# Optimization experiments

Measured on AMD Instinct MI355X. Metric: run time of the kernel, lower is better.

The kernel has to match this reference:

```python
import jax, jax.numpy as jnp
import numpy as np

T = 4096
MOL = 2048
DESC = 6
NSOL = 5
H = 2048
D_BLOCK = MOL + DESC            # 2054
FUSE = D_BLOCK * (1 + NSOL)     # 12324
D_IN = FUSE + 1                 # 12325
BOUNDARY_RF = 0.5
CLAMP_LO, CLAMP_HI = 1e-4, 1.0 - 1e-4


def setup_inputs() -> dict:
    key = jax.random.key(0)
    ks = jax.random.split(key, 32)
    s = 0.02  # weight init scale for numerical stability
    d = {
        "mol_vec": jax.random.normal(ks[0], (MOL,), jnp.float32),
        "solvent_seq": jax.random.uniform(ks[1], (T, NSOL), jnp.float32),
        "desc_seq": jax.random.normal(ks[2], (T, DESC), jnp.float32),
        "rf_true": jax.random.uniform(ks[3], (T,), jnp.float32),
        "solvent_vecs": jax.random.normal(ks[4], (NSOL, MOL), jnp.float32),
    }
    wshapes = [
        ("Wf0", (H, D_IN)), ("Wf1", (H, H)), ("Wf2", (H, H)), ("Wof", (1, H)),
        ("Wb0", (H, D_IN)), ("Wb1", (H, H)), ("Wb2", (H, H)), ("Wob", (1, H)),
    ]
    for i, (name, shp) in enumerate(wshapes):
        d[name] = jax.random.normal(ks[5 + i], shp, jnp.float32) * s
    for name, shp in [("bf0", (H,)), ("bf1", (H,)), ("bf2", (H,)), ("bof", (1,)),
                      ("bb0", (H,)), ("bb1", (H,)), ("bb2", (H,)), ("bob", (1,))]:
        d[name] = jnp.zeros(shp, jnp.float32)
    return d


def _step_features(mol_vec, solvent_seq, desc_seq, solvent_vecs):
    # mol_vec [MOL]; solvent_seq [T,NSOL]; desc_seq [T,DESC]; solvent_vecs [NSOL,MOL]
    mol_cat = jnp.concatenate(
        [jnp.broadcast_to(mol_vec, (T, MOL)), desc_seq], axis=-1)  # [T, D_BLOCK]
    scaled = solvent_seq[:, :, None] * solvent_vecs[None, :, :]      # [T,NSOL,MOL]
    sol_block = jnp.concatenate(
        [scaled, jnp.broadcast_to(desc_seq[:, None, :], (T, NSOL, DESC))], axis=-1)
    sol_flat = sol_block.reshape(T, NSOL * D_BLOCK)
    return jnp.concatenate([mol_cat, sol_flat], axis=-1)             # [T, FUSE]


def _trunk(x, W0, b0, W1, b1, W2, b2):
    # 3 Linear+GELU blocks (dropout is identity in eval)
    h = jax.nn.gelu(x @ W0.T + b0, approximate=False)
    h = jax.nn.gelu(h @ W1.T + b1, approximate=False)
    h = jax.nn.gelu(h @ W2.T + b2, approximate=False)
    return h


def reference(mol_vec, solvent_seq, desc_seq, rf_true, solvent_vecs,
              Wf0, bf0, Wf1, bf1, Wf2, bf2, Wof, bof,
              Wb0, bb0, Wb1, bb1, Wb2, bb2, Wob, bob):
    x = _step_features(mol_vec, solvent_seq, desc_seq, solvent_vecs)  # [T, FUSE]
    rf = jax.lax.stop_gradient(rf_true)  # teacher signal is detached
    b = jnp.asarray([BOUNDARY_RF], dtype=x.dtype)
    prev = jnp.concatenate([b, rf[:-1]])  # fwd branch sees rf_true[t-1]
    nxt = jnp.concatenate([rf[1:], b])    # bwd branch sees rf_true[t+1]

    inp_f = jnp.concatenate([x, prev[:, None]], axis=-1)  # [T, D_IN]
    inp_b = jnp.concatenate([x, nxt[:, None]], axis=-1)

    hf = _trunk(inp_f, Wf0, bf0, Wf1, bf1, Wf2, bf2)
    hb = _trunk(inp_b, Wb0, bb0, Wb1, bb1, Wb2, bb2)
    rf_fwd = (hf @ Wof.T + bof).squeeze(-1)  # [T]
    rf_bwd = (hb @ Wob.T + bob).squeeze(-1)
    rf_fwd = jnp.clip(rf_fwd, CLAMP_LO, CLAMP_HI)
    rf_bwd = jnp.clip(rf_bwd, CLAMP_LO, CLAMP_HI)
    return rf_fwd, rf_bwd
```

## Files before the change

### kernel.cpp

```cpp
#include <hip/hip_runtime.h>
#include <hip/hip_fp16.h>
#include <math.h>

#define T_DIM 4096
#define MOL_N 2048
#define DESC_N 6
#define NSOL_N 5
#define H_DIM 2048
#define DBLK 2054
#define D_IN_N 12325
#define GK 2048

typedef _Float16 f16x8 __attribute__((ext_vector_type(8)));
typedef float f32x4 __attribute__((ext_vector_type(4)));

__device__ __forceinline__ float gelu_f(float x) {
    float v = x * (1.5957691f + 0.0713548f * x * x);
    float e = __expf(-v);
    return x / (1.0f + e);
}

__global__ __launch_bounds__(256) void prep_kernel(
    const float* __restrict__ W1f, const float* __restrict__ W2f,
    const float* __restrict__ W1b, const float* __restrict__ W2b,
    _Float16* __restrict__ Wc,
    const float* __restrict__ W0f, const float* __restrict__ W0b,
    const float* __restrict__ b0f, const float* __restrict__ b0b,
    const float* __restrict__ mol, const float* __restrict__ sv,
    float* __restrict__ fold_f, float* __restrict__ fold_b)
{
    __shared__ float red[4][6];
    const int bid = blockIdx.x;
    const int tid = threadIdx.x;

    if (bid < 16384) {
        const int z = bid >> 12;
        const float* __restrict__ src = (z == 0) ? W1f : (z == 1) ? W2f : (z == 2) ? W1b : W2b;
        _Float16* __restrict__ dst = Wc + (size_t)z * H_DIM * H_DIM;
        const int idx = (bid & 4095) * 256 + tid;
        float4 v = ((const float4*)src)[idx];
        struct h4 { _Float16 a, b, c, d; };
        h4 o;
        o.a = (_Float16)v.x; o.b = (_Float16)v.y; o.c = (_Float16)v.z; o.d = (_Float16)v.w;
        ((h4*)dst)[idx] = o;
        return;
    }

    const int fb = bid - 16384;
    const int h = fb & 2047;
    const int z = fb >> 11;
    const float* __restrict__ W0 = z ? W0b : W0f;
    const float* __restrict__ b0 = z ? b0b : b0f;
    float* __restrict__ fold = z ? fold_b : fold_f;
    const float* __restrict__ row = W0 + (size_t)h * D_IN_N;

    float acc[6] = {0.f, 0.f, 0.f, 0.f, 0.f, 0.f};
    #pragma unroll
    for (int i = 0; i < 8; ++i) {
        const int c = tid + i * 256;
        const float m = mol[c];
        acc[0] += row[c] * m;
        #pragma unroll
        for (int s = 0; s < NSOL_N; ++s)
            acc[1 + s] += row[DBLK * (s + 1) + c] * sv[s * MOL_N + c];
    }
    #pragma unroll
    for (int i = 0; i < 6; ++i) {
        float v = acc[i];
        #pragma unroll
        for (int off = 32; off >= 1; off >>= 1)
            v += __shfl_xor(v, off, 64);
        acc[i] = v;
    }
    const int lane = tid & 63, wave = tid >> 6;
    if (lane == 0) {
        #pragma unroll
        for (int i = 0; i < 6; ++i) red[wave][i] = acc[i];
    }
    __syncthreads();
    if (tid < 6) {
        float s = red[0][tid] + red[1][tid] + red[2][tid] + red[3][tid];
        if (tid == 0) fold[h] = s + b0[h];
        else fold[(size_t)tid * H_DIM + h] = s;
    }
    if (tid >= 64 && tid < 70) {
        int j = tid - 64;
        float w = row[MOL_N + j];
        #pragma unroll
        for (int s = 0; s < NSOL_N; ++s) w += row[DBLK * (s + 1) + MOL_N + j];
        fold[(size_t)(6 + j) * H_DIM + h] = w;
    }
    if (tid == 70) fold[(size_t)12 * H_DIM + h] = row[D_IN_N - 1];
}

__global__ __launch_bounds__(256) void h0_kernel(
    const float* __restrict__ fold_f, const float* __restrict__ fold_b,
    const float* __restrict__ desc, const float* __restrict__ sol,
    const float* __restrict__ rf,
    _Float16* __restrict__ h0f, _Float16* __restrict__ h0b)
{
    const int z = blockIdx.z;
    const float* __restrict__ fold = z ? fold_b : fold_f;
    _Float16* __restrict__ h0 = z ? h0b : h0f;
    const int h = blockIdx.x * 256 + threadIdx.x;
    const int tbase = blockIdx.y * 64;

    const float c0 = fold[h];
    float u[NSOL_N], wd[DESC_N];
    #pragma unroll
    for (int s = 0; s < NSOL_N; ++s) u[s] = fold[(size_t)(1 + s) * H_DIM + h];
    #pragma unroll
    for (int j = 0; j < DESC_N; ++j) wd[j] = fold[(size_t)(6 + j) * H_DIM + h];
    const float wp = fold[(size_t)12 * H_DIM + h];

    for (int i = 0; i < 64; ++i) {
        const int t = tbase + i;
        float pv;
        if (z == 0) pv = (t == 0) ? 0.5f : rf[t - 1];
        else        pv = (t == T_DIM - 1) ? 0.5f : rf[t + 1];
        float pre = c0 + wp * pv;
        #pragma unroll
        for (int s = 0; s < NSOL_N; ++s) pre += u[s] * sol[t * NSOL_N + s];
        #pragma unroll
        for (int j = 0; j < DESC_N; ++j) pre += wd[j] * desc[t * DESC_N + j];
        h0[(size_t)t * H_DIM + h] = (_Float16)gelu_f(pre);
    }
}

__device__ __forceinline__ void gemm_core256(
    const _Float16* __restrict__ A, const _Float16* __restrict__ W,
    const int m0, const int n0, char* sc, f32x4 (&acc)[8][4])
{
    const int tid = threadIdx.x;
    const int wave = tid >> 6;
    const int lane = tid & 63;
    const int t15 = lane & 15;
    const int quad = lane >> 4;
    const int wr = wave >> 2;
    const int wc = wave & 3;
    const int poff = (quad ^ ((t15 >> 1) & 3)) * 16;
    const int aoff0 = (wr * 128 + t15) * 64 + poff;
    const int boff0 = 16384 + (wc * 64 + t15) * 64 + poff;

    const _Float16* gsrc[4];
    #pragma unroll
    for (int ld = 0; ld < 4; ++ld) {
        const int j = (ld & 1) * 512 + tid;
        const int r = j >> 2;
        const int c = (j & 3) ^ ((r >> 1) & 3);
        gsrc[ld] = ((ld < 2) ? (A + (size_t)(m0 + r) * GK)
                             : (W + (size_t)(n0 + r) * GK)) + c * 8;
    }

    #pragma unroll
    for (int mi = 0; mi < 8; ++mi)
        #pragma unroll
        for (int ni = 0; ni < 4; ++ni)
            acc[mi][ni] = (f32x4){0.f, 0.f, 0.f, 0.f};

#define STAGE_T(kt, b) do { \
    char* _db = sc + (b) * 32768; \
    const int _ko = (kt) * 32; \
    __builtin_amdgcn_global_load_lds((const __attribute__((address_space(1))) void*)(gsrc[0] + _ko), (__attribute__((address_space(3))) void*)(_db + wave * 1024), 16, 0, 0); \
    __builtin_amdgcn_global_load_lds((const __attribute__((address_space(1))) void*)(gsrc[1] + _ko), (__attribute__((address_space(3))) void*)(_db + 8192 + wave * 1024), 16, 0, 0); \
    __builtin_amdgcn_global_load_lds((const __attribute__((address_space(1))) void*)(gsrc[2] + _ko), (__attribute__((address_space(3))) void*)(_db + 16384 + wave * 1024), 16, 0, 0); \
    __builtin_amdgcn_global_load_lds((const __attribute__((address_space(1))) void*)(gsrc[3] + _ko), (__attribute__((address_space(3))) void*)(_db + 24576 + wave * 1024), 16, 0, 0); \
} while (0)

#define COMPUTE_T(b) do { \
    const char* _db = sc + (b) * 32768; \
    f16x8 aF[8], bF[4]; \
    _Pragma("unroll") \
    for (int mi = 0; mi < 8; ++mi) aF[mi] = *(const f16x8*)(_db + aoff0 + mi * 1024); \
    _Pragma("unroll") \
    for (int ni = 0; ni < 4; ++ni) bF[ni] = *(const f16x8*)(_db + boff0 + ni * 1024); \
    __builtin_amdgcn_s_setprio(1); \
    _Pragma("unroll") \
    for (int mi = 0; mi < 8; ++mi) { \
        _Pragma("unroll") \
        for (int ni = 0; ni < 4; ++ni) \
            acc[mi][ni] = __builtin_amdgcn_mfma_f32_16x16x32_f16(aF[mi], bF[ni], acc[mi][ni], 0, 0, 0); \
    } \
    __builtin_amdgcn_s_setprio(0); \
    asm volatile("s_waitcnt lgkmcnt(0)" ::: "memory"); \
} while (0)

    STAGE_T(0, 0); STAGE_T(1, 1); STAGE_T(2, 2);

    #pragma unroll 1
    for (int k4 = 0; k4 < 60; k4 += 4) {
        asm volatile("s_waitcnt vmcnt(8)" ::: "memory");
        __builtin_amdgcn_s_barrier();
        STAGE_T(k4 + 3, 3); COMPUTE_T(0);
        asm volatile("s_waitcnt vmcnt(8)" ::: "memory");
        __builtin_amdgcn_s_barrier();
        STAGE_T(k4 + 4, 0); COMPUTE_T(1);
        asm volatile("s_waitcnt vmcnt(8)" ::: "memory");
        __builtin_amdgcn_s_barrier();
        STAGE_T(k4 + 5, 1); COMPUTE_T(2);
        asm volatile("s_waitcnt vmcnt(8)" ::: "memory");
        __builtin_amdgcn_s_barrier();
        STAGE_T(k4 + 6, 2); COMPUTE_T(3);
    }
    asm volatile("s_waitcnt vmcnt(8)" ::: "memory");
    __builtin_amdgcn_s_barrier();
    STAGE_T(63, 3); COMPUTE_T(0);
    asm volatile("s_waitcnt vmcnt(8)" ::: "memory");
    __builtin_amdgcn_s_barrier();
    COMPUTE_T(1);
    asm volatile("s_waitcnt vmcnt(4)" ::: "memory");
    __builtin_amdgcn_s_barrier();
    COMPUTE_T(2);
    asm volatile("s_waitcnt vmcnt(0)" ::: "memory");
    __builtin_amdgcn_s_barrier();
    COMPUTE_T(3);

#undef STAGE_T
#undef COMPUTE_T
}

__global__ __launch_bounds__(512, 2) void gemm1_kernel(
    const _Float16* __restrict__ Af, const _Float16* __restrict__ Ab,
    const _Float16* __restrict__ Wfp, const _Float16* __restrict__ Wbp,
    const float* __restrict__ bfp, const float* __restrict__ bbp,
    _Float16* __restrict__ Cf, _Float16* __restrict__ Cb)
{
    __shared__ _Float16 smem[65536];
    char* sc = (char*)smem;
    const int bid = blockIdx.x;
    const int xcd = bid & 7;
    const int slot = bid >> 3;
    const int z = xcd & 1;
    const int q = xcd >> 1;
    const int m0 = (q * 4 + (slot & 3)) * 256;
    const int n0 = (slot >> 2) * 256;

    const _Float16* __restrict__ A = z ? Ab : Af;
    const _Float16* __restrict__ W = z ? Wbp : Wfp;
    const float* __restrict__ bias = z ? bbp : bfp;
    _Float16* __restrict__ C = z ? Cb : Cf;

    f32x4 acc[8][4];
    gemm_core256(A, W, m0, n0, sc, acc);

    const int tid = threadIdx.x;
    const int wave = tid >> 6, lane = tid & 63;
    const int colC = lane & 15, quad = lane >> 4;
    const int wr = wave >> 2, wc = wave & 3;
    #pragma unroll
    for (int ni = 0; ni < 4; ++ni) {
        const int n = n0 + wc * 64 + ni * 16 + colC;
        const float bv = bias[n];
        #pragma unroll
        for (int mi = 0; mi < 8; ++mi) {
            const int mb = m0 + wr * 128 + mi * 16 + quad * 4;
            #pragma unroll
            for (int r = 0; r < 4; ++r)
                C[(size_t)(mb + r) * H_DIM + n] = (_Float16)gelu_f(acc[mi][ni][r] + bv);
        }
    }
}

__global__ __launch_bounds__(512, 2) void gemm_out_kernel(
    const _Float16* __restrict__ Af, const _Float16* __restrict__ Ab,
    const _Float16* __restrict__ Wfp, const _Float16* __restrict__ Wbp,
    const float* __restrict__ bfp, const float* __restrict__ bbp,
    const float* __restrict__ Wof, const float* __restrict__ Wob,
    float* __restrict__ partial)
{
    __shared__ _Float16 smem[65536];
    char* sc = (char*)smem;
    const int bid = blockIdx.x;
    const int xcd = bid & 7;
    const int slot = bid >> 3;
    const int z = xcd & 1;
    const int q = xcd >> 1;
    const int m0 = (q * 4 + (slot & 3)) * 256;
    const int n0 = (slot >> 2) * 256;

    const _Float16* __restrict__ A = z ? Ab : Af;
    const _Float16* __restrict__ W = z ? Wbp : Wfp;
    const float* __restrict__ bias = z ? bbp : bfp;
    const float* __restrict__ Wo = z ? Wob : Wof;

    f32x4 acc[8][4];
    gemm_core256(A, W, m0, n0, sc, acc);

    const int tid = threadIdx.x;
    const int wave = tid >> 6, lane = tid & 63;
    const int colC = lane & 15, quad = lane >> 4;
    const int wr = wave >> 2, wc = wave & 3;

    float bv[4], wo[4];
    #pragma unroll
    for (int ni = 0; ni < 4; ++ni) {
        const int n = n0 + wc * 64 + ni * 16 + colC;
        bv[ni] = bias[n];
        wo[ni] = Wo[n];
    }

    __syncthreads();
    float* red = (float*)sc;
    #pragma unroll
    for (int mi = 0; mi < 8; ++mi) {
        #pragma unroll
        for (int r = 0; r < 4; ++r) {
            float s = 0.f;
            #pragma unroll
            for (int ni = 0; ni < 4; ++ni)
                s += gelu_f(acc[mi][ni][r] + bv[ni]) * wo[ni];
            s += __shfl_xor(s, 1, 64);
            s += __shfl_xor(s, 2, 64);
            s += __shfl_xor(s, 4, 64);
            s += __shfl_xor(s, 8, 64);
            if (colC == 0)
                red[wc * 256 + wr * 128 + mi * 16 + quad * 4 + r] = s;
        }
    }
    __syncthreads();
    if (tid < 256) {
        float v = red[tid] + red[256 + tid] + red[512 + tid] + red[768 + tid];
        const int n_tile = slot >> 2;
        partial[((size_t)z * 8 + n_tile) * T_DIM + m0 + tid] = v;
    }
}

__global__ __launch_bounds__(256) void finalize_kernel(
    const float* __restrict__ partial,
    const float* __restrict__ bof, const float* __restrict__ bob,
    float* __restrict__ out)
{
    const int idx = blockIdx.x * 256 + threadIdx.x;
    const int z = idx >> 12;
    const int row = idx & 4095;
    float v = z ? bob[0] : bof[0];
    #pragma unroll
    for (int nt = 0; nt < 8; ++nt)
        v += partial[((size_t)z * 8 + nt) * T_DIM + row];
    v = fminf(fmaxf(v, 1e-4f), 1.0f - 1e-4f);
    out[idx] = v;
}

extern "C" void kernel_launch(void* const* d_in, const int* in_sizes, int n_in,
                              void* d_out, int out_size, void* d_ws, size_t ws_size,
                              hipStream_t stream)
{
    (void)in_sizes; (void)n_in; (void)out_size; (void)ws_size;
    const float* mol = (const float*)d_in[0];
    const float* sol = (const float*)d_in[1];
    const float* desc = (const float*)d_in[2];
    const float* rf  = (const float*)d_in[3];
    const float* sv  = (const float*)d_in[4];
    const float* Wf0 = (const float*)d_in[5];
    const float* Wf1 = (const float*)d_in[6];
    const float* Wf2 = (const float*)d_in[7];
    const float* Wof = (const float*)d_in[8];
    const float* Wb0 = (const float*)d_in[9];
    const float* Wb1 = (const float*)d_in[10];
    const float* Wb2 = (const float*)d_in[11];
    const float* Wob = (const float*)d_in[12];
    const float* bf0 = (const float*)d_in[13];
    const float* bf1 = (const float*)d_in[14];
    const float* bf2 = (const float*)d_in[15];
    const float* bof = (const float*)d_in[16];
    const float* bb0 = (const float*)d_in[17];
    const float* bb1 = (const float*)d_in[18];
    const float* bb2 = (const float*)d_in[19];
    const float* bob = (const float*)d_in[20];
    float* out = (float*)d_out;

    char* ws = (char*)d_ws;
    float* fold_f = (float*)(ws + 0);
    float* fold_b = (float*)(ws + 131072);
    _Float16* Wc = (_Float16*)(ws + 262144);
    const size_t WSZ = (size_t)H_DIM * H_DIM;
    _Float16* W1f_c = Wc;
    _Float16* W2f_c = Wc + WSZ;
    _Float16* W1b_c = Wc + 2 * WSZ;
    _Float16* W2b_c = Wc + 3 * WSZ;
    const size_t HSZ = (size_t)T_DIM * H_DIM;
    _Float16* h0f = (_Float16*)(ws + 33816576);
    _Float16* h0b = h0f + HSZ;
    _Float16* h1f = (_Float16*)(ws + 33816576 + 2 * 16777216);
    _Float16* h1b = h1f + HSZ;
    float* partial = (float*)(ws + 33816576);

    prep_kernel<<<dim3(20480), 256, 0, stream>>>(
        Wf1, Wf2, Wb1, Wb2, Wc, Wf0, Wb0, bf0, bb0, mol, sv, fold_f, fold_b);
    h0_kernel<<<dim3(8, 64, 2), 256, 0, stream>>>(fold_f, fold_b, desc, sol, rf, h0f, h0b);
    gemm1_kernel<<<dim3(256), 512, 0, stream>>>(h0f, h0b, W1f_c, W1b_c, bf1, bb1, h1f, h1b);
    gemm_out_kernel<<<dim3(256), 512, 0, stream>>>(h1f, h1b, W2f_c, W2b_c, bf2, bb2, Wof, Wob, partial);
    finalize_kernel<<<dim3(32), 256, 0, stream>>>(partial, bof, bob, out);
}
```

Baseline: 465.8 us.

## Split prep into LDS-staged W0 fold kernel and separate fp16 convert kernel

The combined prep kernel is split in two. A fold kernel streams each W0 row into LDS using global_load_lds with 16-byte chunks, handling rows of 12325 floats that are not 16-byte aligned, and processes four rows per block. A separate convert kernel casts W1/W2 to fp16 with four float4 loads per thread. The h0 kernel now computes four hidden units per thread, using vectorized fold loads and 4-wide fp16 stores. The goal is better load coalescing and more memory-level parallelism in these bandwidth-bound preprocessing stages, at the cost of one extra kernel launch and 53KB of LDS per fold block, which limits occupancy.

```diff
diff --git a/kernel.cpp b/kernel.cpp
--- a/kernel.cpp
+++ b/kernel.cpp
@@ -20,77 +20,103 @@
     return x / (1.0f + e);
 }
 
-__global__ __launch_bounds__(256) void prep_kernel(
-    const float* __restrict__ W1f, const float* __restrict__ W2f,
-    const float* __restrict__ W1b, const float* __restrict__ W2b,
-    _Float16* __restrict__ Wc,
+__global__ __launch_bounds__(256) void fold2_kernel(
     const float* __restrict__ W0f, const float* __restrict__ W0b,
     const float* __restrict__ b0f, const float* __restrict__ b0b,
     const float* __restrict__ mol, const float* __restrict__ sv,
     float* __restrict__ fold_f, float* __restrict__ fold_b)
 {
+    __shared__ float wrow[13312];
     __shared__ float red[4][6];
-    const int bid = blockIdx.x;
     const int tid = threadIdx.x;
-
-    if (bid < 16384) {
-        const int z = bid >> 12;
-        const float* __restrict__ src = (z == 0) ? W1f : (z == 1) ? W2f : (z == 2) ? W1b : W2b;
-        _Float16* __restrict__ dst = Wc + (size_t)z * H_DIM * H_DIM;
-        const int idx = (bid & 4095) * 256 + tid;
-        float4 v = ((const float4*)src)[idx];
-        struct h4 { _Float16 a, b, c, d; };
+    const int wave = tid >> 6, lane = tid & 63;
+    const size_t matbytes = (size_t)2048 * D_IN_N * 4;
+    char* wrc = (char*)wrow;
+
+    for (int rr = 0; rr < 4; ++rr) {
+        const int r = blockIdx.x + rr * 1024;
+        const int z = r >> 11, h = r & 2047;
+        const float* __restrict__ W0 = z ? W0b : W0f;
+        const float* __restrict__ b0 = z ? b0b : b0f;
+        float* __restrict__ fold = z ? fold_b : fold_f;
+        const size_t rowdw = (size_t)h * D_IN_N;
+        const size_t A0 = rowdw & ~(size_t)3;
+        const int p = (int)(rowdw & 3);
+        const size_t A0byte = A0 * 4;
+        const char* __restrict__ W0c = (const char*)W0;
+
+        #pragma unroll
+        for (int j = 0; j < 13; ++j) {
+            const size_t off = (size_t)j * 4096 + (size_t)wave * 1024 + (size_t)lane * 16;
+            size_t g = A0byte + off;
+            if (g + 16 > matbytes) g = A0byte;
+            __builtin_amdgcn_global_load_lds(
+                (const __attribute__((address_space(1))) void*)(W0c + g),
+                (__attribute__((address_space(3))) void*)(wrc + off), 16, 0, 0);
+        }
+        asm volatile("s_waitcnt vmcnt(0)" ::: "memory");
+        __syncthreads();
+
+        float acc[6] = {0.f, 0.f, 0.f, 0.f, 0.f, 0.f};
+        #pragma unroll
+        for (int s = 0; s < 6; ++s) {
+            const int cb = (s == 0) ? 0 : DBLK * s;
+            const float* __restrict__ xp = (s == 0) ? mol : (sv + (size_t)(s - 1) * MOL_N);
+            #pragma unroll
+            for (int q = 0; q < 8; ++q) {
+                const int col = tid + q * 256;
+                acc[s] += wrow[p + cb + col] * xp[col];
+            }
+        }
+        #pragma unroll
+        for (int i = 0; i < 6; ++i) {
+            float v = acc[i];
+            #pragma unroll
+            for (int off = 32; off >= 1; off >>= 1)
+                v += __shfl_xor(v, off, 64);
+            acc[i] = v;
+        }
+        if (lane == 0) {
+            #pragma unroll
+            for (int i = 0; i < 6; ++i) red[wave][i] = acc[i];
+        }
+        __syncthreads();
+        if (tid < 6) {
+            float s = red[0][tid] + red[1][tid] + red[2][tid] + red[3][tid];
+            if (tid == 0) fold[h] = s + b0[h];
+            else fold[(size_t)tid * H_DIM + h] = s;
+        }
+        if (tid >= 64 && tid < 70) {
+            const int j = tid - 64;
+            float w = wrow[p + MOL_N + j];
+            #pragma unroll
+            for (int s = 1; s <= 5; ++s) w += wrow[p + DBLK * s + MOL_N + j];
+            fold[(size_t)(6 + j) * H_DIM + h] = w;
+        }
+        if (tid == 70) fold[(size_t)12 * H_DIM + h] = wrow[p + D_IN_N - 1];
+        __syncthreads();
+    }
+}
+
+__global__ __launch_bounds__(256) void conv_kernel(
+    const float* __restrict__ W1f, const float* __restrict__ W2f,
+    const float* __restrict__ W1b, const float* __restrict__ W2b,
+    _Float16* __restrict__ Wc)
+{
+    const int b = blockIdx.x;
+    const int z = b >> 10;
+    const float* __restrict__ src = (z == 0) ? W1f : (z == 1) ? W2f : (z == 2) ? W1b : W2b;
+    _Float16* __restrict__ dst = Wc + (size_t)z * H_DIM * H_DIM;
+    const int base4 = (b & 1023) * 1024;
+    struct h4 { _Float16 a, b, c, d; };
+    #pragma unroll
+    for (int k = 0; k < 4; ++k) {
+        const int i4 = base4 + k * 256 + threadIdx.x;
+        float4 v = ((const float4*)src)[i4];
         h4 o;
         o.a = (_Float16)v.x; o.b = (_Float16)v.y; o.c = (_Float16)v.z; o.d = (_Float16)v.w;
-        ((h4*)dst)[idx] = o;
-        return;
-    }
-
-    const int fb = bid - 16384;
-    const int h = fb & 2047;
-    const int z = fb >> 11;
-    const float* __restrict__ W0 = z ? W0b : W0f;
-    const float* __restrict__ b0 = z ? b0b : b0f;
-    float* __restrict__ fold = z ? fold_b : fold_f;
-    const float* __restrict__ row = W0 + (size_t)h * D_IN_N;
-
-    float acc[6] = {0.f, 0.f, 0.f, 0.f, 0.f, 0.f};
-    #pragma unroll
-    for (int i = 0; i < 8; ++i) {
-        const int c = tid + i * 256;
-        const float m = mol[c];
-        acc[0] += row[c] * m;
-        #pragma unroll
-        for (int s = 0; s < NSOL_N; ++s)
-            acc[1 + s] += row[DBLK * (s + 1) + c] * sv[s * MOL_N + c];
-    }
-    #pragma unroll
-    for (int i = 0; i < 6; ++i) {
-        float v = acc[i];
-        #pragma unroll
-        for (int off = 32; off >= 1; off >>= 1)
-            v += __shfl_xor(v, off, 64);
-        acc[i] = v;
-    }
-    const int lane = tid & 63, wave = tid >> 6;
-    if (lane == 0) {
-        #pragma unroll
-        for (int i = 0; i < 6; ++i) red[wave][i] = acc[i];
-    }
-    __syncthreads();
-    if (tid < 6) {
-        float s = red[0][tid] + red[1][tid] + red[2][tid] + red[3][tid];
-        if (tid == 0) fold[h] = s + b0[h];
-        else fold[(size_t)tid * H_DIM + h] = s;
-    }
-    if (tid >= 64 && tid < 70) {
-        int j = tid - 64;
-        float w = row[MOL_N + j];
-        #pragma unroll
-        for (int s = 0; s < NSOL_N; ++s) w += row[DBLK * (s + 1) + MOL_N + j];
-        fold[(size_t)(6 + j) * H_DIM + h] = w;
-    }
-    if (tid == 70) fold[(size_t)12 * H_DIM + h] = row[D_IN_N - 1];
+        ((h4*)dst)[i4] = o;
+    }
 }
 
 __global__ __launch_bounds__(256) void h0_kernel(
@@ -102,28 +128,52 @@
     const int z = blockIdx.z;
     const float* __restrict__ fold = z ? fold_b : fold_f;
     _Float16* __restrict__ h0 = z ? h0b : h0f;
-    const int h = blockIdx.x * 256 + threadIdx.x;
+    const int hb = blockIdx.x * 1024 + threadIdx.x * 4;
     const int tbase = blockIdx.y * 64;
 
-    const float c0 = fold[h];
-    float u[NSOL_N], wd[DESC_N];
-    #pragma unroll
-    for (int s = 0; s < NSOL_N; ++s) u[s] = fold[(size_t)(1 + s) * H_DIM + h];
-    #pragma unroll
-    for (int j = 0; j < DESC_N; ++j) wd[j] = fold[(size_t)(6 + j) * H_DIM + h];
-    const float wp = fold[(size_t)12 * H_DIM + h];
-
+    float c0a[4], wpa[4], ua[NSOL_N][4], wda[DESC_N][4];
+    {
+        float4 v = *(const float4*)&fold[hb];
+        c0a[0] = v.x; c0a[1] = v.y; c0a[2] = v.z; c0a[3] = v.w;
+        v = *(const float4*)&fold[(size_t)12 * H_DIM + hb];
+        wpa[0] = v.x; wpa[1] = v.y; wpa[2] = v.z; wpa[3] = v.w;
+        #pragma unroll
+        for (int s = 0; s < NSOL_N; ++s) {
+            v = *(const float4*)&fold[(size_t)(1 + s) * H_DIM + hb];
+            ua[s][0] = v.x; ua[s][1] = v.y; ua[s][2] = v.z; ua[s][3] = v.w;
+        }
+        #pragma unroll
+        for (int j = 0; j < DESC_N; ++j) {
+            v = *(const float4*)&fold[(size_t)(6 + j) * H_DIM + hb];
+            wda[j][0] = v.x; wda[j][1] = v.y; wda[j][2] = v.z; wda[j][3] = v.w;
+        }
+    }
+
+    struct h4s { _Float16 a, b, c, d; };
     for (int i = 0; i < 64; ++i) {
         const int t = tbase + i;
         float pv;
         if (z == 0) pv = (t == 0) ? 0.5f : rf[t - 1];
         else        pv = (t == T_DIM - 1) ? 0.5f : rf[t + 1];
-        float pre = c0 + wp * pv;
-        #pragma unroll
-        for (int s = 0; s < NSOL_N; ++s) pre += u[s] * sol[t * NSOL_N + s];
-        #pragma unroll
-        for (int j = 0; j < DESC_N; ++j) pre += wd[j] * desc[t * DESC_N + j];
-        h0[(size_t)t * H_DIM + h] = (_Float16)gelu_f(pre);
+        float sl[NSOL_N], dc[DESC_N];
+        #pragma unroll
+        for (int s = 0; s < NSOL_N; ++s) sl[s] = sol[t * NSOL_N + s];
+        #pragma unroll
+        for (int j = 0; j < DESC_N; ++j) dc[j] = desc[t * DESC_N + j];
+        float o[4];
+        #pragma unroll
+        for (int e = 0; e < 4; ++e) {
+            float pre = c0a[e] + wpa[e] * pv;
+            #pragma unroll
+            for (int s = 0; s < NSOL_N; ++s) pre += ua[s][e] * sl[s];
+            #pragma unroll
+            for (int j = 0; j < DESC_N; ++j) pre += wda[j][e] * dc[j];
+            o[e] = gelu_f(pre);
+        }
+        h4s ov;
+        ov.a = (_Float16)o[0]; ov.b = (_Float16)o[1];
+        ov.c = (_Float16)o[2]; ov.d = (_Float16)o[3];
+        *(h4s*)&h0[(size_t)t * H_DIM + hb] = ov;
     }
 }
 
@@ -385,9 +435,9 @@
     _Float16* h1b = h1f + HSZ;
     float* partial = (float*)(ws + 33816576);
 
-    prep_kernel<<<dim3(20480), 256, 0, stream>>>(
-        Wf1, Wf2, Wb1, Wb2, Wc, Wf0, Wb0, bf0, bb0, mol, sv, fold_f, fold_b);
-    h0_kernel<<<dim3(8, 64, 2), 256, 0, stream>>>(fold_f, fold_b, desc, sol, rf, h0f, h0b);
+    fold2_kernel<<<dim3(1024), 256, 0, stream>>>(Wf0, Wb0, bf0, bb0, mol, sv, fold_f, fold_b);
+    conv_kernel<<<dim3(4096), 256, 0, stream>>>(Wf1, Wf2, Wb1, Wb2, Wc);
+    h0_kernel<<<dim3(2, 64, 2), 256, 0, stream>>>(fold_f, fold_b, desc, sol, rf, h0f, h0b);
     gemm1_kernel<<<dim3(256), 512, 0, stream>>>(h0f, h0b, W1f_c, W1b_c, bf1, bb1, h1f, h1b);
     gemm_out_kernel<<<dim3(256), 512, 0, stream>>>(h1f, h1b, W2f_c, W2b_c, bf2, bb2, Wof, Wob, partial);
     finalize_kernel<<<dim3(32), 256, 0, stream>>>(partial, bof, bob, out);
```

Measured after the change: 469.8 us. About the same (+0.8%).
